# Optimization experiments

Hardware: AMD Instinct MI355X
Metric: run time of the kernel (lower is better)

## Reference

```python
import jax, jax.numpy as jnp
import numpy as np

B, SQ, SKV, D = 4, 4096, 4096, 64

def setup_inputs() -> dict:
    key = jax.random.key(0)
    kq, kv = jax.random.split(key)
    query = jax.random.normal(kq, (B, SQ, D), dtype=jnp.float32)
    value = jax.random.normal(kv, (B, SKV, D), dtype=jnp.float32)
    return {"query": query, "value": value}

def reference(query, value):
    # scores = Q @ V^T  (value acts as both keys and values; no 1/sqrt(d) scaling)
    scores = jnp.einsum('bqd,bkd->bqk', query, value)  # [B, SQ, SKV]
    dist = jax.nn.softmax(scores, axis=-1)
    context = jnp.einsum('bqk,bkd->bqd', dist, value)  # [B, SQ, D]
    return context
```

## Files before the change

kernel.cpp:

```cpp
#include <hip/hip_runtime.h>


#define NB   4
#define SQ   4096
#define SKV  4096
#define DH   64
#define L2E  1.44269504088896340736f

typedef _Float16 half8 __attribute__((ext_vector_type(8)));
typedef _Float16 half4 __attribute__((ext_vector_type(4)));
typedef _Float16 half2v __attribute__((ext_vector_type(2)));
typedef float f32x4 __attribute__((ext_vector_type(4)));
typedef unsigned short u16;

#define MFMA16(a, b, c) __builtin_amdgcn_mfma_f32_16x16x16f16((a), (b), (c), 0, 0, 0)
#define MFMA32(a, b, c) __builtin_amdgcn_mfma_f32_16x16x32_f16((a), (b), (c), 0, 0, 0)

__device__ __forceinline__ u16 f2h(float f) {
  _Float16 h = (_Float16)f;
  return __builtin_bit_cast(u16, h);
}
__device__ __forceinline__ half2v pkrtz(float a, float b) {
  return __builtin_bit_cast(half2v, __builtin_amdgcn_cvt_pkrtz(a, b));
}

typedef __attribute__((address_space(1))) void gvoid;
typedef __attribute__((address_space(3))) void lvoid;
__device__ __forceinline__ void dma16(const u16* g, u16* l) {
  __builtin_amdgcn_global_load_lds((gvoid*)g, (lvoid*)l, 16, 0, 0);
}

__global__ __launch_bounds__(256) void prep_kernel(
    const float* __restrict__ V, u16* __restrict__ vh, u16* __restrict__ vt) {
  __shared__ u16 ldsT[16 * 72];
  int blk = blockIdx.x;
  int b   = blk >> 8;
  int rem = blk & 255;
  int j0  = (rem >> 2) << 6;
  int d0  = (rem & 3) << 4;
  int t   = threadIdx.x;
  int j   = t >> 2;
  int dc  = (t & 3) << 2;

  const float* src = V + ((size_t)(b * SKV) + j0 + j) * DH + d0 + dc;
  float4 v4 = *(const float4*)src;
  u16 h[4] = {f2h(v4.x), f2h(v4.y), f2h(v4.z), f2h(v4.w)};
  unsigned p0 = (unsigned)h[0] | ((unsigned)h[1] << 16);
  unsigned p1 = (unsigned)h[2] | ((unsigned)h[3] << 16);
  int dfull = d0 + dc;
  int physd = ((((dfull >> 3) ^ (j & 7)) << 3)) + (dfull & 7);
  *(uint2*)(vh + ((size_t)(b * SKV) + j0 + j) * DH + physd) = make_uint2(p0, p1);

#pragma unroll
  for (int k = 0; k < 4; ++k) ldsT[(dc + k) * 72 + j] = h[k];
  __syncthreads();

  int dl = t >> 4;
  int jc = (t & 15) << 2;
  u16 tr[4];
#pragma unroll
  for (int k = 0; k < 4; ++k) tr[k] = ldsT[dl * 72 + jc + k];
  unsigned q0 = (unsigned)tr[0] | ((unsigned)tr[1] << 16);
  unsigned q1 = (unsigned)tr[2] | ((unsigned)tr[3] << 16);
  int d   = d0 + dl;
  int kc2 = jc >> 5;
  int g   = (jc >> 4) & 1;
  int qd  = (jc >> 2) & 3;
  int hp  = ((kc2 << 2) | qd) ^ (d & 7);
  *(uint2*)(vt + ((size_t)(b * DH) + d) * SKV + j0 + (hp << 3) + (g << 2)) =
      make_uint2(q0, q1);
}

__global__ __launch_bounds__(256, 4) void attn_kernel(
    const float* __restrict__ Q,
    const u16* __restrict__ vh,
    const u16* __restrict__ vt,
    u16* __restrict__ po,
    float* __restrict__ pm,
    float* __restrict__ pl,
    int S, int kvLen) {
  __shared__ __align__(16) u16 lds[2][2][4096];

  int blk  = blockIdx.x;
  int tile = blk / S;
  int s    = blk - tile * S;
  int b    = tile >> 6;
  int q0   = (tile & 63) << 6;
  int kv0  = s * kvLen;
  int t    = threadIdx.x;
  int wave = t >> 6;
  int lane = t & 63;
  int col  = lane & 15;
  int quad = lane >> 4;
  int qw   = q0 + (wave << 4);
  int c7   = col & 7;

  const u16* gv  = vh + (size_t)(b * SKV) * DH;
  const u16* gvt = vt + (size_t)(b * DH) * SKV;

  int r0 = t >> 3;
  int c0 = (t & 7) << 3;
  int wb = wave << 9;

  half8 qf[2];
#pragma unroll
  for (int kc = 0; kc < 2; ++kc) {
    const float* qp = Q + ((size_t)(b * SQ) + qw + col) * DH + kc * 32 + (quad << 3);
    float4 a0 = *(const float4*)qp;
    float4 a1 = *(const float4*)(qp + 4);
    half8 hq;
    hq[0] = (_Float16)(a0.x * L2E); hq[1] = (_Float16)(a0.y * L2E);
    hq[2] = (_Float16)(a0.z * L2E); hq[3] = (_Float16)(a0.w * L2E);
    hq[4] = (_Float16)(a1.x * L2E); hq[5] = (_Float16)(a1.y * L2E);
    hq[6] = (_Float16)(a1.z * L2E); hq[7] = (_Float16)(a1.w * L2E);
    qf[kc] = hq;
  }

  f32x4 o[4];
#pragma unroll
  for (int nf = 0; nf < 4; ++nf) o[nf] = (f32x4){0.f, 0.f, 0.f, 0.f};
  float m_r = -1e30f, l_r = 0.f;

  dma16(gv + ((size_t)(kv0 + r0) << 6) + c0,       &lds[0][0][0] + wb);
  dma16(gv + ((size_t)(kv0 + r0 + 32) << 6) + c0,  &lds[0][0][0] + 2048 + wb);
  dma16(gvt + (size_t)r0 * SKV + kv0 + c0,         &lds[0][1][0] + wb);
  dma16(gvt + (size_t)(r0 + 32) * SKV + kv0 + c0,  &lds[0][1][0] + 2048 + wb);

  int nIter = kvLen >> 6;
  int cur = 0;
  for (int it = 0; it < nIter; ++it) {
    __syncthreads();

    if ((it + 1) < nIter) {
      int j0n = kv0 + ((it + 1) << 6);
      u16* dv  = &lds[cur ^ 1][0][0];
      u16* dvt = &lds[cur ^ 1][1][0];
      dma16(gv + ((size_t)(j0n + r0) << 6) + c0,      dv + wb);
      dma16(gv + ((size_t)(j0n + r0 + 32) << 6) + c0, dv + 2048 + wb);
      dma16(gvt + (size_t)r0 * SKV + j0n + c0,        dvt + wb);
      dma16(gvt + (size_t)(r0 + 32) * SKV + j0n + c0, dvt + 2048 + wb);
    }

    const u16* sv = &lds[cur][0][0];
    const u16* st = &lds[cur][1][0];

    f32x4 sf[4];
#pragma unroll
    for (int nf = 0; nf < 4; ++nf) sf[nf] = (f32x4){0.f, 0.f, 0.f, 0.f};
#pragma unroll
    for (int nf = 0; nf < 4; ++nf) {
#pragma unroll
      for (int kc = 0; kc < 2; ++kc) {
        int ch = ((kc << 2) | quad) ^ c7;
        half8 av = *(const half8*)(sv + ((nf * 16 + col) << 6) + (ch << 3));
        sf[nf] = MFMA32(av, qf[kc], sf[nf]);
      }
    }

    half4 pf[4];
    {
      float tm = sf[0][0];
#pragma unroll
      for (int nf = 0; nf < 4; ++nf)
#pragma unroll
        for (int r = 0; r < 4; ++r) tm = fmaxf(tm, sf[nf][r]);
      tm = fmaxf(tm, __shfl_xor(tm, 16, 64));
      tm = fmaxf(tm, __shfl_xor(tm, 32, 64));
      float mn = fmaxf(m_r, tm);
      float al = exp2f(m_r - mn);
      m_r = mn;
      float rs = 0.f;
#pragma unroll
      for (int nf = 0; nf < 4; ++nf) {
        float p0 = exp2f(sf[nf][0] - mn);
        float p1 = exp2f(sf[nf][1] - mn);
        float p2 = exp2f(sf[nf][2] - mn);
        float p3 = exp2f(sf[nf][3] - mn);
        rs += (p0 + p1) + (p2 + p3);
        half2v lo = pkrtz(p0, p1);
        half2v hi = pkrtz(p2, p3);
        pf[nf] = __builtin_shufflevector(lo, hi, 0, 1, 2, 3);
      }
      l_r = l_r * al + rs;
#pragma unroll
      for (int nf = 0; nf < 4; ++nf)
#pragma unroll
        for (int r = 0; r < 4; ++r) o[nf][r] *= al;
    }

#pragma unroll
    for (int kc2 = 0; kc2 < 2; ++kc2) {
#pragma unroll
      for (int nf2 = 0; nf2 < 4; ++nf2) {
        int ch = ((kc2 << 2) | quad) ^ c7;
        half8 w8 = *(const half8*)(st + ((nf2 * 16 + col) << 6) + (ch << 3));
        half4 wlo = __builtin_shufflevector(w8, w8, 0, 1, 2, 3);
        half4 whi = __builtin_shufflevector(w8, w8, 4, 5, 6, 7);
        o[nf2] = MFMA16(wlo, pf[kc2 * 2], o[nf2]);
        o[nf2] = MFMA16(whi, pf[kc2 * 2 + 1], o[nf2]);
      }
    }

    cur ^= 1;
  }

  l_r += __shfl_xor(l_r, 16, 64);
  l_r += __shfl_xor(l_r, 32, 64);
  int pidx = tile * S + s;
  if (quad == 0) {
    pm[(size_t)pidx * 64 + (wave << 4) + col] = m_r;
    pl[(size_t)pidx * 64 + (wave << 4) + col] = l_r;
  }

  __syncthreads();
  u16* tp = &lds[0][0][0];
  {
    int qrow = (wave << 4) + col;
#pragma unroll
    for (int nf2 = 0; nf2 < 4; ++nf2) {
#pragma unroll
      for (int r2 = 0; r2 < 4; r2 += 2) {
        unsigned pk = (unsigned)f2h(o[nf2][r2]) |
                      ((unsigned)f2h(o[nf2][r2 + 1]) << 16);
        int d = nf2 * 16 + (quad << 2) + r2;
        *(unsigned*)(tp + qrow * 72 + d) = pk;
      }
    }
  }
  __syncthreads();
  {
    u16* pob = po + (size_t)pidx * 64 * 64;
    int q = t >> 2, hc = (t & 3) << 4;
    uint4 x0 = *(const uint4*)(tp + q * 72 + hc);
    uint4 x1 = *(const uint4*)(tp + q * 72 + hc + 8);
    *(uint4*)(pob + q * 64 + hc)     = x0;
    *(uint4*)(pob + q * 64 + hc + 8) = x1;
  }
}

__global__ __launch_bounds__(256) void combine_kernel(
    const u16* __restrict__ po,
    const float* __restrict__ pm,
    const float* __restrict__ pl,
    float* __restrict__ out, int S) {
  int t    = threadIdx.x;
  int rowg = blockIdx.x * 32 + (t >> 3);
  int tile = rowg >> 6;
  int row  = rowg & 63;
  int dc   = (t & 7) << 3;

  float mv[8], lv[8];
  float M = -1e30f;
  for (int s = 0; s < S; ++s) {
    mv[s] = pm[(size_t)(tile * S + s) * 64 + row];
    lv[s] = pl[(size_t)(tile * S + s) * 64 + row];
    M = fmaxf(M, mv[s]);
  }
  float L = 0.f, w[8];
  for (int s = 0; s < S; ++s) {
    w[s] = exp2f(mv[s] - M);
    L += lv[s] * w[s];
  }
  float acc[8] = {0.f, 0.f, 0.f, 0.f, 0.f, 0.f, 0.f, 0.f};
  for (int s = 0; s < S; ++s) {
    const u16* p = po + (size_t)(tile * S + s) * 4096 + row * 64 + dc;
    uint4 raw = *(const uint4*)p;
    half8 x = __builtin_bit_cast(half8, raw);
#pragma unroll
    for (int k = 0; k < 8; ++k) acc[k] += w[s] * (float)x[k];
  }
  float invL = 1.0f / L;
  float* op = out + (size_t)rowg * 64 + dc;
  f32x4 o0 = (f32x4){acc[0], acc[1], acc[2], acc[3]};
  f32x4 o1 = (f32x4){acc[4], acc[5], acc[6], acc[7]};
  *(f32x4*)op       = o0 * invL;
  *(f32x4*)(op + 4) = o1 * invL;
}

extern "C" void kernel_launch(void* const* d_in, const int* in_sizes, int n_in,
                              void* d_out, int out_size, void* d_ws, size_t ws_size,
                              hipStream_t stream) {
  const float* Q = (const float*)d_in[0];
  const float* V = (const float*)d_in[1];
  float* out = (float*)d_out;

  const size_t convBytes = (size_t)2 * NB * SKV * DH * 2;
  auto partBytes = [](int S) {
    return (size_t)NB * 64 * S * ((size_t)64 * 64 * 2 + 64 * 8);
  };
  int S = 4;
  while (S > 1 && ws_size < convBytes + partBytes(S)) S >>= 1;
  int kvLen = SKV / S;

  u16* vh = (u16*)d_ws;
  u16* vt = vh + (size_t)NB * SKV * DH;
  u16* po = vt + (size_t)NB * SKV * DH;
  float* pm = (float*)(po + (size_t)NB * 64 * S * 64 * 64);
  float* pl = pm + (size_t)NB * 64 * S * 64;

  prep_kernel<<<NB * 256, 256, 0, stream>>>(V, vh, vt);
  attn_kernel<<<NB * 64 * S, 256, 0, stream>>>(Q, vh, vt, po, pm, pl, S, kvLen);
  combine_kernel<<<NB * SQ / 32, 256, 0, stream>>>(po, pm, pl, out, S);
}
```

Measured before the change: 106.0 us.

## Fuse V fp16 conversion and transpose into attention kernel staging

Removes the separate prep kernel that converted V to fp16 and wrote swizzled row-major and transposed copies to global memory. The attention kernel now loads fp32 V tiles into registers, converts them, and writes both swizzled layouts into LDS itself, prefetching the next tile into registers during compute. This drops one kernel launch and the extra global round trip for the converted copies. In exchange, each attention block redoes the conversion for every KV tile it reads, fp32 loads double the global traffic per tile, and the asynchronous global-to-LDS DMA is replaced by register staging plus scattered 16-bit LDS stores for the transpose, which may cause bank conflicts and add register pressure.

```diff
diff --git a/kernel.cpp b/kernel.cpp
--- a/kernel.cpp
+++ b/kernel.cpp
@@ -24,57 +24,9 @@
   return __builtin_bit_cast(half2v, __builtin_amdgcn_cvt_pkrtz(a, b));
 }
 
-typedef __attribute__((address_space(1))) void gvoid;
-typedef __attribute__((address_space(3))) void lvoid;
-__device__ __forceinline__ void dma16(const u16* g, u16* l) {
-  __builtin_amdgcn_global_load_lds((gvoid*)g, (lvoid*)l, 16, 0, 0);
-}
-
-__global__ __launch_bounds__(256) void prep_kernel(
-    const float* __restrict__ V, u16* __restrict__ vh, u16* __restrict__ vt) {
-  __shared__ u16 ldsT[16 * 72];
-  int blk = blockIdx.x;
-  int b   = blk >> 8;
-  int rem = blk & 255;
-  int j0  = (rem >> 2) << 6;
-  int d0  = (rem & 3) << 4;
-  int t   = threadIdx.x;
-  int j   = t >> 2;
-  int dc  = (t & 3) << 2;
-
-  const float* src = V + ((size_t)(b * SKV) + j0 + j) * DH + d0 + dc;
-  float4 v4 = *(const float4*)src;
-  u16 h[4] = {f2h(v4.x), f2h(v4.y), f2h(v4.z), f2h(v4.w)};
-  unsigned p0 = (unsigned)h[0] | ((unsigned)h[1] << 16);
-  unsigned p1 = (unsigned)h[2] | ((unsigned)h[3] << 16);
-  int dfull = d0 + dc;
-  int physd = ((((dfull >> 3) ^ (j & 7)) << 3)) + (dfull & 7);
-  *(uint2*)(vh + ((size_t)(b * SKV) + j0 + j) * DH + physd) = make_uint2(p0, p1);
-
-#pragma unroll
-  for (int k = 0; k < 4; ++k) ldsT[(dc + k) * 72 + j] = h[k];
-  __syncthreads();
-
-  int dl = t >> 4;
-  int jc = (t & 15) << 2;
-  u16 tr[4];
-#pragma unroll
-  for (int k = 0; k < 4; ++k) tr[k] = ldsT[dl * 72 + jc + k];
-  unsigned q0 = (unsigned)tr[0] | ((unsigned)tr[1] << 16);
-  unsigned q1 = (unsigned)tr[2] | ((unsigned)tr[3] << 16);
-  int d   = d0 + dl;
-  int kc2 = jc >> 5;
-  int g   = (jc >> 4) & 1;
-  int qd  = (jc >> 2) & 3;
-  int hp  = ((kc2 << 2) | qd) ^ (d & 7);
-  *(uint2*)(vt + ((size_t)(b * DH) + d) * SKV + j0 + (hp << 3) + (g << 2)) =
-      make_uint2(q0, q1);
-}
-
 __global__ __launch_bounds__(256, 4) void attn_kernel(
     const float* __restrict__ Q,
-    const u16* __restrict__ vh,
-    const u16* __restrict__ vt,
+    const float* __restrict__ V,
     u16* __restrict__ po,
     float* __restrict__ pm,
     float* __restrict__ pl,
@@ -93,14 +45,30 @@
   int col  = lane & 15;
   int quad = lane >> 4;
   int qw   = q0 + (wave << 4);
-  int c7   = col & 7;
-
-  const u16* gv  = vh + (size_t)(b * SKV) * DH;
-  const u16* gvt = vt + (size_t)(b * DH) * SKV;
-
-  int r0 = t >> 3;
-  int c0 = (t & 7) << 3;
-  int wb = wave << 9;
+  int c7   = col & 15 & 7;
+
+  const float* gV = V + (size_t)(b * SKV) * DH;
+
+  int sr = t >> 2;
+  int sdc = (t & 3) << 4;
+  int sk = sr & 7;
+  int sH   = (((sr >> 5) << 2) | ((sr >> 2) & 3));
+  int srem = (((sr >> 4) & 1) << 2) + (sr & 3);
+
+  auto stage_write = [&](u16* dv, u16* dvt, const float4 f[4]) {
+    u16 h[16];
+#pragma unroll
+    for (int i = 0; i < 4; ++i) {
+      h[i * 4 + 0] = f2h(f[i].x); h[i * 4 + 1] = f2h(f[i].y);
+      h[i * 4 + 2] = f2h(f[i].z); h[i * 4 + 3] = f2h(f[i].w);
+    }
+    int c0 = sdc >> 3;
+    *(uint4*)(dv + (sr << 6) + (((c0)     ^ sk) << 3)) = *(const uint4*)(h);
+    *(uint4*)(dv + (sr << 6) + (((c0 + 1) ^ sk) << 3)) = *(const uint4*)(h + 8);
+#pragma unroll
+    for (int i = 0; i < 16; ++i)
+      dvt[((sdc + i) << 6) + ((sH ^ (i & 7)) << 3) + srem] = h[i];
+  };
 
   half8 qf[2];
 #pragma unroll
@@ -121,24 +89,26 @@
   for (int nf = 0; nf < 4; ++nf) o[nf] = (f32x4){0.f, 0.f, 0.f, 0.f};
   float m_r = -1e30f, l_r = 0.f;
 
-  dma16(gv + ((size_t)(kv0 + r0) << 6) + c0,       &lds[0][0][0] + wb);
-  dma16(gv + ((size_t)(kv0 + r0 + 32) << 6) + c0,  &lds[0][0][0] + 2048 + wb);
-  dma16(gvt + (size_t)r0 * SKV + kv0 + c0,         &lds[0][1][0] + wb);
-  dma16(gvt + (size_t)(r0 + 32) * SKV + kv0 + c0,  &lds[0][1][0] + 2048 + wb);
+  {
+    const float* src = gV + (size_t)(kv0 + sr) * DH + sdc;
+    float4 f[4] = {((const float4*)src)[0], ((const float4*)src)[1],
+                   ((const float4*)src)[2], ((const float4*)src)[3]};
+    stage_write(&lds[0][0][0], &lds[0][1][0], f);
+  }
 
   int nIter = kvLen >> 6;
   int cur = 0;
   for (int it = 0; it < nIter; ++it) {
     __syncthreads();
 
-    if ((it + 1) < nIter) {
-      int j0n = kv0 + ((it + 1) << 6);
-      u16* dv  = &lds[cur ^ 1][0][0];
-      u16* dvt = &lds[cur ^ 1][1][0];
-      dma16(gv + ((size_t)(j0n + r0) << 6) + c0,      dv + wb);
-      dma16(gv + ((size_t)(j0n + r0 + 32) << 6) + c0, dv + 2048 + wb);
-      dma16(gvt + (size_t)r0 * SKV + j0n + c0,        dvt + wb);
-      dma16(gvt + (size_t)(r0 + 32) * SKV + j0n + c0, dvt + 2048 + wb);
+    float4 f[4];
+    bool more = (it + 1) < nIter;
+    if (more) {
+      const float* src = gV + (size_t)(kv0 + ((it + 1) << 6) + sr) * DH + sdc;
+      f[0] = ((const float4*)src)[0];
+      f[1] = ((const float4*)src)[1];
+      f[2] = ((const float4*)src)[2];
+      f[3] = ((const float4*)src)[3];
     }
 
     const u16* sv = &lds[cur][0][0];
@@ -201,6 +171,7 @@
       }
     }
 
+    if (more) stage_write(&lds[cur ^ 1][0][0], &lds[cur ^ 1][1][0], f);
     cur ^= 1;
   }
 
@@ -284,21 +255,17 @@
   const float* V = (const float*)d_in[1];
   float* out = (float*)d_out;
 
-  const size_t convBytes = (size_t)2 * NB * SKV * DH * 2;
   auto partBytes = [](int S) {
     return (size_t)NB * 64 * S * ((size_t)64 * 64 * 2 + 64 * 8);
   };
   int S = 4;
-  while (S > 1 && ws_size < convBytes + partBytes(S)) S >>= 1;
+  while (S > 1 && ws_size < partBytes(S)) S >>= 1;
   int kvLen = SKV / S;
 
-  u16* vh = (u16*)d_ws;
-  u16* vt = vh + (size_t)NB * SKV * DH;
-  u16* po = vt + (size_t)NB * SKV * DH;
+  u16* po = (u16*)d_ws;
   float* pm = (float*)(po + (size_t)NB * 64 * S * 64 * 64);
   float* pl = pm + (size_t)NB * 64 * S * 64;
 
-  prep_kernel<<<NB * 256, 256, 0, stream>>>(V, vh, vt);
-  attn_kernel<<<NB * 64 * S, 256, 0, stream>>>(Q, vh, vt, po, pm, pl, S, kvLen);
+  attn_kernel<<<NB * 64 * S, 256, 0, stream>>>(Q, V, po, pm, pl, S, kvLen);
   combine_kernel<<<NB * SQ / 32, 256, 0, stream>>>(po, pm, pl, out, S);
 }
```

Result: slower. 108.3 us (+2.1%).
